# Optimization experiments

Hardware: AMD Instinct MI355X
Metric: run time of the kernel (lower is better)

Reference implementation:

```python
import jax, jax.numpy as jnp
import numpy as np

B, L, D = 4, 4096, 128
WINDOW = 64
NEG = -1e9
LN_EPS = 1e-5


def setup_inputs() -> dict:
    key = jax.random.key(0)
    ks = jax.random.split(key, 6)
    x = jax.random.normal(ks[0], (B, L, D), dtype=jnp.float32)
    # windowed adjacency with self-loops: adj[b,i,j]=1 iff |i-j| <= WINDOW
    idx = jnp.arange(L)
    band = (jnp.abs(idx[:, None] - idx[None, :]) <= WINDOW).astype(jnp.int32)
    adj = jnp.broadcast_to(band, (B, L, L))
    mask = np.ones((B, L), dtype=np.int32)
    mask[B // 2 :, -L // 8 :] = 0
    mask = jnp.asarray(mask)
    s = 1.0 / np.sqrt(D)
    Wq = jax.random.normal(ks[1], (D, D), dtype=jnp.float32) * s
    Wk = jax.random.normal(ks[2], (D, D), dtype=jnp.float32) * s
    Wv = jax.random.normal(ks[3], (D, D), dtype=jnp.float32) * s
    W_upd = jax.random.normal(ks[4], (2 * D, D), dtype=jnp.float32) * (1.0 / np.sqrt(2 * D))
    b_upd = jnp.zeros((D,), dtype=jnp.float32)
    gamma = jnp.ones((D,), dtype=jnp.float32)
    beta = jnp.zeros((D,), dtype=jnp.float32)
    return {"x": x, "adj": adj, "mask": mask, "Wq": Wq, "Wk": Wk, "Wv": Wv,
            "W_upd": W_upd, "b_upd": b_upd, "gamma": gamma, "beta": beta}


def reference(x, adj, mask, Wq, Wk, Wv, W_upd, b_upd, gamma, beta):
    d = x.shape[-1]
    q = jnp.einsum("bld,de->ble", x, Wq)
    k = jnp.einsum("bld,de->ble", x, Wk)
    v = jnp.einsum("bld,de->ble", x, Wv)
    logits = jnp.einsum("bld,bmd->blm", q, k) / jnp.sqrt(jnp.float32(d))
    logits = jnp.where(adj == 0, NEG, logits)
    logits = jnp.where(mask[:, :, None] == 0, NEG, logits)
    logits = jnp.where(mask[:, None, :] == 0, NEG, logits)
    attn = jax.nn.softmax(logits, axis=-1)  # dropout = identity (eval mode)
    agg = jnp.einsum("blm,bmd->bld", attn, v)
    h = jnp.concatenate([x, agg], axis=-1)  # [B, L, 2D]
    upd = jax.nn.relu(h @ W_upd + b_upd)
    y = x + upd
    mu = jnp.mean(y, axis=-1, keepdims=True)
    var = jnp.var(y, axis=-1, keepdims=True)
    return gamma * (y - mu) * jax.lax.rsqrt(var + LN_EPS) + beta
```

## Files before the change

kernel.cpp:

```cpp
#include <hip/hip_runtime.h>

#define BB 4
#define LL 4096
#define DD 128
#define WIN 64
#define BL (BB * LL)

#define TQ 32
#define CK 64

typedef unsigned short u16;

__device__ __forceinline__ u16 f2b(float f) {
  union { float f; unsigned int u; } x;
  x.f = f;
  unsigned int r = x.u + 0x7fffu + ((x.u >> 16) & 1u);
  return (u16)(r >> 16);
}
__device__ __forceinline__ float b2f_lo(unsigned int u) {
  union { unsigned int u; float f; } x;
  x.u = u << 16;
  return x.f;
}
__device__ __forceinline__ float b2f_hi(unsigned int u) {
  union { unsigned int u; float f; } x;
  x.u = u & 0xffff0000u;
  return x.f;
}
__device__ __forceinline__ void unpack8(uint4 u, float* f) {
  f[0] = b2f_lo(u.x); f[1] = b2f_hi(u.x);
  f[2] = b2f_lo(u.y); f[3] = b2f_hi(u.y);
  f[4] = b2f_lo(u.z); f[5] = b2f_hi(u.z);
  f[6] = b2f_lo(u.w); f[7] = b2f_hi(u.w);
}

__global__ __launch_bounds__(256) void qkv_kernel(
    const float* __restrict__ x, const float* __restrict__ Wq,
    const float* __restrict__ Wk, const float* __restrict__ Wv,
    u16* __restrict__ q, u16* __restrict__ k, u16* __restrict__ v,
    float* __restrict__ vmean_sum) {
  __shared__ float xs[32][132];
  __shared__ float ws[32][132];

  const int t = threadIdx.x;
  const int row0 = blockIdx.x * 32;
  const int tm = t >> 4;
  const int tn = t & 15;

  {
    int rr = t >> 5, d4 = t & 31;
    const float4* xg = (const float4*)(x + (size_t)row0 * DD);
    #pragma unroll
    for (int p = 0; p < 4; ++p) {
      int row = p * 8 + rr;
      ((float4*)&xs[row][0])[d4] = xg[row * 32 + d4];
    }
  }

  const float* Ws[3] = {Wq, Wk, Wv};
  u16* outs[3] = {q, k, v};

  for (int w = 0; w < 3; ++w) {
    float acc0[8], acc1[8];
    #pragma unroll
    for (int j = 0; j < 8; ++j) { acc0[j] = 0.f; acc1[j] = 0.f; }

    for (int kc = 0; kc < 4; ++kc) {
      __syncthreads();
      {
        int rr = t >> 5, d4 = t & 31;
        const float4* wg = (const float4*)(Ws[w] + (size_t)kc * 32 * DD);
        #pragma unroll
        for (int p = 0; p < 4; ++p) {
          int row = p * 8 + rr;
          ((float4*)&ws[row][0])[d4] = wg[row * 32 + d4];
        }
      }
      __syncthreads();

      #pragma unroll
      for (int k4 = 0; k4 < 8; ++k4) {
        float4 a0 = ((const float4*)&xs[tm][0])[kc * 8 + k4];
        float4 a1 = ((const float4*)&xs[tm + 16][0])[kc * 8 + k4];
        float a0c[4] = {a0.x, a0.y, a0.z, a0.w};
        float a1c[4] = {a1.x, a1.y, a1.z, a1.w};
        #pragma unroll
        for (int o = 0; o < 4; ++o) {
          int kk = k4 * 4 + o;
          float4 b0 = ((const float4*)&ws[kk][0])[tn];
          float4 b1 = ((const float4*)&ws[kk][0])[16 + tn];
          acc0[0] += a0c[o] * b0.x; acc0[1] += a0c[o] * b0.y;
          acc0[2] += a0c[o] * b0.z; acc0[3] += a0c[o] * b0.w;
          acc0[4] += a0c[o] * b1.x; acc0[5] += a0c[o] * b1.y;
          acc0[6] += a0c[o] * b1.z; acc0[7] += a0c[o] * b1.w;
          acc1[0] += a1c[o] * b0.x; acc1[1] += a1c[o] * b0.y;
          acc1[2] += a1c[o] * b0.z; acc1[3] += a1c[o] * b0.w;
          acc1[4] += a1c[o] * b1.x; acc1[5] += a1c[o] * b1.y;
          acc1[6] += a1c[o] * b1.z; acc1[7] += a1c[o] * b1.w;
        }
      }
    }

    u16* op = outs[w] + (size_t)row0 * DD;
    {
      ushort4 s;
      s.x = f2b(acc0[0]); s.y = f2b(acc0[1]); s.z = f2b(acc0[2]); s.w = f2b(acc0[3]);
      *(ushort4*)(op + (size_t)tm * DD + 4 * tn) = s;
      s.x = f2b(acc0[4]); s.y = f2b(acc0[5]); s.z = f2b(acc0[6]); s.w = f2b(acc0[7]);
      *(ushort4*)(op + (size_t)tm * DD + 64 + 4 * tn) = s;
      s.x = f2b(acc1[0]); s.y = f2b(acc1[1]); s.z = f2b(acc1[2]); s.w = f2b(acc1[3]);
      *(ushort4*)(op + (size_t)(tm + 16) * DD + 4 * tn) = s;
      s.x = f2b(acc1[4]); s.y = f2b(acc1[5]); s.z = f2b(acc1[6]); s.w = f2b(acc1[7]);
      *(ushort4*)(op + (size_t)(tm + 16) * DD + 64 + 4 * tn) = s;
    }

    if (w == 2) {
      __syncthreads();
      ((float4*)&ws[tm][0])[tn] = make_float4(acc0[0], acc0[1], acc0[2], acc0[3]);
      ((float4*)&ws[tm][0])[16 + tn] = make_float4(acc0[4], acc0[5], acc0[6], acc0[7]);
      ((float4*)&ws[tm + 16][0])[tn] = make_float4(acc1[0], acc1[1], acc1[2], acc1[3]);
      ((float4*)&ws[tm + 16][0])[16 + tn] = make_float4(acc1[4], acc1[5], acc1[6], acc1[7]);
      __syncthreads();
      if (t < DD) {
        float s = 0.f;
        #pragma unroll 8
        for (int r = 0; r < 32; ++r) s += ws[r][t];
        atomicAdd(&vmean_sum[(row0 >> 12) * DD + t], s);
      }
    }
  }
}

__global__ __launch_bounds__(128) void attn_kernel(
    const u16* __restrict__ q, const u16* __restrict__ k,
    const u16* __restrict__ v, const float* __restrict__ vmean_sum,
    const int* __restrict__ mask, float* __restrict__ agg) {
  __shared__ u16 qs[TQ][136];
  __shared__ u16 ks[CK][136];
  __shared__ float ps[TQ][66];
  __shared__ int cms[CK];

  const int bx = blockIdx.x;
  const int b = bx >> 7;
  const int i0 = (bx & 127) * TQ;
  const int t = threadIdx.x;
  const int tm = t >> 4;
  const int tn = t & 15;

  const size_t rowbase = ((size_t)b * LL + i0) * DD;

  {
    const uint4* qg = (const uint4*)(q + rowbase);
    #pragma unroll
    for (int p = 0; p < 4; ++p) {
      int row = p * 8 + tm;
      *(uint4*)&qs[row][8 * tn] = qg[row * 16 + tn];
    }
  }

  float accv[4][8];
  float lsum[4];
  #pragma unroll
  for (int m = 0; m < 4; ++m) {
    lsum[m] = 0.f;
    #pragma unroll
    for (int j = 0; j < 8; ++j) accv[m][j] = 0.f;
  }

  for (int ch = 0; ch < 3; ++ch) {
    const int j0 = i0 - WIN + ch * CK;
    __syncthreads();

    {
      #pragma unroll
      for (int p = 0; p < 8; ++p) {
        int row = p * 8 + tm;
        int j = j0 + row;
        int jc = j < 0 ? 0 : (j > LL - 1 ? LL - 1 : j);
        *(uint4*)&ks[row][8 * tn] =
            ((const uint4*)(k + ((size_t)b * LL + jc) * DD))[tn];
      }
      if (t < CK) {
        int j = j0 + t;
        cms[t] = (j >= 0 && j < LL) ? mask[b * LL + j] : 0;
      }
    }
    __syncthreads();

    float S[4][4];
    #pragma unroll
    for (int m = 0; m < 4; ++m)
      #pragma unroll
      for (int n = 0; n < 4; ++n) S[m][n] = 0.f;

    for (int k8 = 0; k8 < 16; ++k8) {
      float af[4][8], bf[4][8];
      #pragma unroll
      for (int m = 0; m < 4; ++m)
        unpack8(*(const uint4*)&qs[tm + 8 * m][8 * k8], af[m]);
      #pragma unroll
      for (int n = 0; n < 4; ++n)
        unpack8(*(const uint4*)&ks[tn + 16 * n][8 * k8], bf[n]);
      #pragma unroll
      for (int m = 0; m < 4; ++m)
        #pragma unroll
        for (int n = 0; n < 4; ++n) {
          float s = S[m][n];
          #pragma unroll
          for (int j = 0; j < 8; ++j) s += af[m][j] * bf[n][j];
          S[m][n] = s;
        }
    }

    #pragma unroll
    for (int m = 0; m < 4; ++m) {
      int iR = i0 + tm + 8 * m;
      #pragma unroll
      for (int n = 0; n < 4; ++n) {
        int col = tn + 16 * n;
        int j = j0 + col;
        int dj = iR - j;
        dj = dj < 0 ? -dj : dj;
        bool ok = (dj <= WIN) && ((unsigned)j < (unsigned)LL) && (cms[col] != 0);
        float p = ok ? __expf(S[m][n] * 0.08838834764831845f) : 0.f;
        lsum[m] += p;
        ps[tm + 8 * m][col] = p;
      }
    }
    __syncthreads();

    {
      #pragma unroll
      for (int p = 0; p < 8; ++p) {
        int row = p * 8 + tm;
        int j = j0 + row;
        int jc = j < 0 ? 0 : (j > LL - 1 ? LL - 1 : j);
        *(uint4*)&ks[row][8 * tn] =
            ((const uint4*)(v + ((size_t)b * LL + jc) * DD))[tn];
      }
    }
    __syncthreads();

    #pragma unroll 2
    for (int c = 0; c < CK; ++c) {
      float vf[8];
      unpack8(*(const uint4*)&ks[c][8 * tn], vf);
      float pm[4];
      #pragma unroll
      for (int m = 0; m < 4; ++m) pm[m] = ps[tm + 8 * m][c];
      #pragma unroll
      for (int m = 0; m < 4; ++m)
        #pragma unroll
        for (int j = 0; j < 8; ++j) accv[m][j] += pm[m] * vf[j];
    }
  }

  #pragma unroll
  for (int m = 0; m < 4; ++m) {
    float l = lsum[m];
    l += __shfl_xor(l, 1);
    l += __shfl_xor(l, 2);
    l += __shfl_xor(l, 4);
    l += __shfl_xor(l, 8);
    lsum[m] = l;
  }

  #pragma unroll
  for (int m = 0; m < 4; ++m) {
    int row = tm + 8 * m;
    int iR = i0 + row;
    float o[8];
    if (mask[b * LL + iR] != 0) {
      float inv = 1.0f / lsum[m];
      #pragma unroll
      for (int j = 0; j < 8; ++j) o[j] = accv[m][j] * inv;
    } else {
      const float s = 1.0f / LL;
      #pragma unroll
      for (int j = 0; j < 8; ++j) o[j] = vmean_sum[b * DD + 8 * tn + j] * s;
    }
    float* dst = agg + rowbase + (size_t)row * DD + 8 * tn;
    *(float4*)dst = make_float4(o[0], o[1], o[2], o[3]);
    *(float4*)(dst + 4) = make_float4(o[4], o[5], o[6], o[7]);
  }
}

__global__ __launch_bounds__(256) void mlp_ln_kernel(
    const float* __restrict__ x, const float* __restrict__ agg,
    const float* __restrict__ Wu, const float* __restrict__ bias,
    const float* __restrict__ gamma, const float* __restrict__ beta,
    float* __restrict__ out) {
  __shared__ float hs[32][36];
  __shared__ float ws[32][132];

  const int t = threadIdx.x;
  const int row0 = blockIdx.x * 32;
  const int tm = t >> 4, tn = t & 15;

  float acc0[8], acc1[8];
  #pragma unroll
  for (int j = 0; j < 8; ++j) { acc0[j] = 0.f; acc1[j] = 0.f; }

  for (int kc = 0; kc < 8; ++kc) {
    __syncthreads();
    {
      const float* src = (kc < 4) ? (x + (size_t)row0 * DD + kc * 32)
                                  : (agg + (size_t)row0 * DD + (kc - 4) * 32);
      int row = t >> 3, d4 = t & 7;
      ((float4*)&hs[row][0])[d4] = ((const float4*)(src + (size_t)row * DD))[d4];
    }
    {
      int rr = t >> 5, d4 = t & 31;
      const float4* wg = (const float4*)(Wu + (size_t)kc * 32 * DD);
      #pragma unroll
      for (int p = 0; p < 4; ++p) {
        int row = p * 8 + rr;
        ((float4*)&ws[row][0])[d4] = wg[row * 32 + d4];
      }
    }
    __syncthreads();

    #pragma unroll
    for (int k4 = 0; k4 < 8; ++k4) {
      float4 a0 = ((const float4*)&hs[tm][0])[k4];
      float4 a1 = ((const float4*)&hs[tm + 16][0])[k4];
      float a0c[4] = {a0.x, a0.y, a0.z, a0.w};
      float a1c[4] = {a1.x, a1.y, a1.z, a1.w};
      #pragma unroll
      for (int o = 0; o < 4; ++o) {
        int kk = k4 * 4 + o;
        float4 b0 = ((const float4*)&ws[kk][0])[tn];
        float4 b1 = ((const float4*)&ws[kk][0])[16 + tn];
        acc0[0] += a0c[o] * b0.x; acc0[1] += a0c[o] * b0.y;
        acc0[2] += a0c[o] * b0.z; acc0[3] += a0c[o] * b0.w;
        acc0[4] += a0c[o] * b1.x; acc0[5] += a0c[o] * b1.y;
        acc0[6] += a0c[o] * b1.z; acc0[7] += a0c[o] * b1.w;
        acc1[0] += a1c[o] * b0.x; acc1[1] += a1c[o] * b0.y;
        acc1[2] += a1c[o] * b0.z; acc1[3] += a1c[o] * b0.w;
        acc1[4] += a1c[o] * b1.x; acc1[5] += a1c[o] * b1.y;
        acc1[6] += a1c[o] * b1.z; acc1[7] += a1c[o] * b1.w;
      }
    }
  }

  const float4 bv0 = ((const float4*)bias)[tn];
  const float4 bv1 = ((const float4*)bias)[16 + tn];
  const float4 g0 = ((const float4*)gamma)[tn];
  const float4 g1 = ((const float4*)gamma)[16 + tn];
  const float4 be0 = ((const float4*)beta)[tn];
  const float4 be1 = ((const float4*)beta)[16 + tn];

  #pragma unroll
  for (int m = 0; m < 2; ++m) {
    const float* accp0 = m ? acc1 : acc0;
    int row = tm + 16 * m;
    const float4 xr0 = ((const float4*)(x + (size_t)(row0 + row) * DD))[tn];
    const float4 xr1 = ((const float4*)(x + (size_t)(row0 + row) * DD))[16 + tn];
    float y[8];
    y[0] = xr0.x + fmaxf(accp0[0] + bv0.x, 0.f);
    y[1] = xr0.y + fmaxf(accp0[1] + bv0.y, 0.f);
    y[2] = xr0.z + fmaxf(accp0[2] + bv0.z, 0.f);
    y[3] = xr0.w + fmaxf(accp0[3] + bv0.w, 0.f);
    y[4] = xr1.x + fmaxf(accp0[4] + bv1.x, 0.f);
    y[5] = xr1.y + fmaxf(accp0[5] + bv1.y, 0.f);
    y[6] = xr1.z + fmaxf(accp0[6] + bv1.z, 0.f);
    y[7] = xr1.w + fmaxf(accp0[7] + bv1.w, 0.f);
    float s = 0.f, ss = 0.f;
    #pragma unroll
    for (int j = 0; j < 8; ++j) { s += y[j]; ss += y[j] * y[j]; }
    s += __shfl_xor(s, 1); ss += __shfl_xor(ss, 1);
    s += __shfl_xor(s, 2); ss += __shfl_xor(ss, 2);
    s += __shfl_xor(s, 4); ss += __shfl_xor(ss, 4);
    s += __shfl_xor(s, 8); ss += __shfl_xor(ss, 8);
    float mu = s * (1.0f / DD);
    float var = ss * (1.0f / DD) - mu * mu;
    float rstd = rsqrtf(var + 1e-5f);
    float4 o0 = make_float4(g0.x * ((y[0] - mu) * rstd) + be0.x,
                            g0.y * ((y[1] - mu) * rstd) + be0.y,
                            g0.z * ((y[2] - mu) * rstd) + be0.z,
                            g0.w * ((y[3] - mu) * rstd) + be0.w);
    float4 o1 = make_float4(g1.x * ((y[4] - mu) * rstd) + be1.x,
                            g1.y * ((y[5] - mu) * rstd) + be1.y,
                            g1.z * ((y[6] - mu) * rstd) + be1.z,
                            g1.w * ((y[7] - mu) * rstd) + be1.w);
    ((float4*)(out + (size_t)(row0 + row) * DD))[tn] = o0;
    ((float4*)(out + (size_t)(row0 + row) * DD))[16 + tn] = o1;
  }
}

extern "C" void kernel_launch(void* const* d_in, const int* in_sizes, int n_in,
                              void* d_out, int out_size, void* d_ws,
                              size_t ws_size, hipStream_t stream) {
  const float* x = (const float*)d_in[0];
  const int* mask = (const int*)d_in[2];
  const float* Wq = (const float*)d_in[3];
  const float* Wk = (const float*)d_in[4];
  const float* Wv = (const float*)d_in[5];
  const float* Wu = (const float*)d_in[6];
  const float* bias = (const float*)d_in[7];
  const float* gamma = (const float*)d_in[8];
  const float* beta = (const float*)d_in[9];
  float* out = (float*)d_out;

  float* agg = (float*)d_ws;
  u16* q = (u16*)(agg + (size_t)BL * DD);
  u16* k = q + (size_t)BL * DD;
  u16* v = k + (size_t)BL * DD;
  float* vmean_sum = (float*)(v + (size_t)BL * DD);

  hipMemsetAsync(vmean_sum, 0, BB * DD * sizeof(float), stream);

  qkv_kernel<<<BL / 32, 256, 0, stream>>>(x, Wq, Wk, Wv, q, k, v, vmean_sum);
  attn_kernel<<<BL / TQ, 128, 0, stream>>>(q, k, v, vmean_sum, mask, agg);
  mlp_ln_kernel<<<BL / 32, 256, 0, stream>>>(x, agg, Wu, bias, gamma, beta,
                                             out);
}
```

Before: 429.9 us.

## Restructure QKV, attention and MLP kernels to read weights directly and stage K/V together

The QKV kernel now launches one grid slice per projection over 64-row tiles and reads weights straight from global memory (through cache) instead of staging them in shared memory. The attention kernel loads K and V into separate shared buffers in a single pass and stores probabilities transposed, cutting one sync and one reload per chunk. The MLP/LayerNorm kernel stages the full concatenated [x, agg] row block once and also reads weights from global memory. This removes shared-memory weight tiling and the barriers around it. In exchange it relies on L1/L2 for weight reuse and uses more shared memory per attention block.

```diff
diff --git a/kernel.cpp b/kernel.cpp
--- a/kernel.cpp
+++ b/kernel.cpp
@@ -5,9 +5,7 @@
 #define DD 128
 #define WIN 64
 #define BL (BB * LL)
-
 #define TQ 32
-#define CK 64
 
 typedef unsigned short u16;
 
@@ -33,100 +31,81 @@
   f[4] = b2f_lo(u.z); f[5] = b2f_hi(u.z);
   f[6] = b2f_lo(u.w); f[7] = b2f_hi(u.w);
 }
+__device__ __forceinline__ float comp4(float4 a, int d) {
+  return d == 0 ? a.x : (d == 1 ? a.y : (d == 2 ? a.z : a.w));
+}
 
 __global__ __launch_bounds__(256) void qkv_kernel(
     const float* __restrict__ x, const float* __restrict__ Wq,
     const float* __restrict__ Wk, const float* __restrict__ Wv,
     u16* __restrict__ q, u16* __restrict__ k, u16* __restrict__ v,
     float* __restrict__ vmean_sum) {
-  __shared__ float xs[32][132];
-  __shared__ float ws[32][132];
+  __shared__ float xs[64][132];
 
   const int t = threadIdx.x;
-  const int row0 = blockIdx.x * 32;
-  const int tm = t >> 4;
-  const int tn = t & 15;
+  const int row0 = blockIdx.x * 64;
+  const int which = blockIdx.y;
+  const float* __restrict__ W = which == 0 ? Wq : (which == 1 ? Wk : Wv);
+  u16* __restrict__ outp = which == 0 ? q : (which == 1 ? k : v);
 
   {
-    int rr = t >> 5, d4 = t & 31;
     const float4* xg = (const float4*)(x + (size_t)row0 * DD);
     #pragma unroll
-    for (int p = 0; p < 4; ++p) {
-      int row = p * 8 + rr;
-      ((float4*)&xs[row][0])[d4] = xg[row * 32 + d4];
-    }
-  }
-
-  const float* Ws[3] = {Wq, Wk, Wv};
-  u16* outs[3] = {q, k, v};
-
-  for (int w = 0; w < 3; ++w) {
-    float acc0[8], acc1[8];
-    #pragma unroll
-    for (int j = 0; j < 8; ++j) { acc0[j] = 0.f; acc1[j] = 0.f; }
-
-    for (int kc = 0; kc < 4; ++kc) {
-      __syncthreads();
-      {
-        int rr = t >> 5, d4 = t & 31;
-        const float4* wg = (const float4*)(Ws[w] + (size_t)kc * 32 * DD);
-        #pragma unroll
-        for (int p = 0; p < 4; ++p) {
-          int row = p * 8 + rr;
-          ((float4*)&ws[row][0])[d4] = wg[row * 32 + d4];
-        }
-      }
-      __syncthreads();
-
-      #pragma unroll
-      for (int k4 = 0; k4 < 8; ++k4) {
-        float4 a0 = ((const float4*)&xs[tm][0])[kc * 8 + k4];
-        float4 a1 = ((const float4*)&xs[tm + 16][0])[kc * 8 + k4];
-        float a0c[4] = {a0.x, a0.y, a0.z, a0.w};
-        float a1c[4] = {a1.x, a1.y, a1.z, a1.w};
-        #pragma unroll
-        for (int o = 0; o < 4; ++o) {
-          int kk = k4 * 4 + o;
-          float4 b0 = ((const float4*)&ws[kk][0])[tn];
-          float4 b1 = ((const float4*)&ws[kk][0])[16 + tn];
-          acc0[0] += a0c[o] * b0.x; acc0[1] += a0c[o] * b0.y;
-          acc0[2] += a0c[o] * b0.z; acc0[3] += a0c[o] * b0.w;
-          acc0[4] += a0c[o] * b1.x; acc0[5] += a0c[o] * b1.y;
-          acc0[6] += a0c[o] * b1.z; acc0[7] += a0c[o] * b1.w;
-          acc1[0] += a1c[o] * b0.x; acc1[1] += a1c[o] * b0.y;
-          acc1[2] += a1c[o] * b0.z; acc1[3] += a1c[o] * b0.w;
-          acc1[4] += a1c[o] * b1.x; acc1[5] += a1c[o] * b1.y;
-          acc1[6] += a1c[o] * b1.z; acc1[7] += a1c[o] * b1.w;
-        }
-      }
-    }
-
-    u16* op = outs[w] + (size_t)row0 * DD;
-    {
-      ushort4 s;
-      s.x = f2b(acc0[0]); s.y = f2b(acc0[1]); s.z = f2b(acc0[2]); s.w = f2b(acc0[3]);
-      *(ushort4*)(op + (size_t)tm * DD + 4 * tn) = s;
-      s.x = f2b(acc0[4]); s.y = f2b(acc0[5]); s.z = f2b(acc0[6]); s.w = f2b(acc0[7]);
-      *(ushort4*)(op + (size_t)tm * DD + 64 + 4 * tn) = s;
-      s.x = f2b(acc1[0]); s.y = f2b(acc1[1]); s.z = f2b(acc1[2]); s.w = f2b(acc1[3]);
-      *(ushort4*)(op + (size_t)(tm + 16) * DD + 4 * tn) = s;
-      s.x = f2b(acc1[4]); s.y = f2b(acc1[5]); s.z = f2b(acc1[6]); s.w = f2b(acc1[7]);
-      *(ushort4*)(op + (size_t)(tm + 16) * DD + 64 + 4 * tn) = s;
-    }
-
-    if (w == 2) {
-      __syncthreads();
-      ((float4*)&ws[tm][0])[tn] = make_float4(acc0[0], acc0[1], acc0[2], acc0[3]);
-      ((float4*)&ws[tm][0])[16 + tn] = make_float4(acc0[4], acc0[5], acc0[6], acc0[7]);
-      ((float4*)&ws[tm + 16][0])[tn] = make_float4(acc1[0], acc1[1], acc1[2], acc1[3]);
-      ((float4*)&ws[tm + 16][0])[16 + tn] = make_float4(acc1[4], acc1[5], acc1[6], acc1[7]);
-      __syncthreads();
-      if (t < DD) {
-        float s = 0.f;
-        #pragma unroll 8
-        for (int r = 0; r < 32; ++r) s += ws[r][t];
-        atomicAdd(&vmean_sum[(row0 >> 12) * DD + t], s);
-      }
+    for (int p = 0; p < 8; ++p) {
+      int idx = t + 256 * p;
+      ((float4*)&xs[idx >> 5][0])[idx & 31] = xg[idx];
+    }
+  }
+  __syncthreads();
+
+  const int rg = t >> 5;
+  const int cg = t & 31;
+  const float4* W4 = (const float4*)W;
+
+  float4 acc[8];
+  #pragma unroll
+  for (int m = 0; m < 8; ++m) acc[m] = make_float4(0.f, 0.f, 0.f, 0.f);
+
+  #pragma unroll 2
+  for (int k4 = 0; k4 < 32; ++k4) {
+    float4 a[8];
+    #pragma unroll
+    for (int m = 0; m < 8; ++m)
+      a[m] = ((const float4*)&xs[rg + 8 * m][0])[k4];
+    #pragma unroll
+    for (int d = 0; d < 4; ++d) {
+      float4 w = W4[(size_t)(k4 * 4 + d) * 32 + cg];
+      #pragma unroll
+      for (int m = 0; m < 8; ++m) {
+        float av = comp4(a[m], d);
+        acc[m].x += av * w.x; acc[m].y += av * w.y;
+        acc[m].z += av * w.z; acc[m].w += av * w.w;
+      }
+    }
+  }
+
+  #pragma unroll
+  for (int m = 0; m < 8; ++m) {
+    ushort4 s;
+    s.x = f2b(acc[m].x); s.y = f2b(acc[m].y);
+    s.z = f2b(acc[m].z); s.w = f2b(acc[m].w);
+    *(ushort4*)(outp + (size_t)(row0 + rg + 8 * m) * DD + 4 * cg) = s;
+  }
+
+  if (which == 2) {
+    __syncthreads();
+    float4 cs = make_float4(0.f, 0.f, 0.f, 0.f);
+    #pragma unroll
+    for (int m = 0; m < 8; ++m) {
+      cs.x += acc[m].x; cs.y += acc[m].y; cs.z += acc[m].z; cs.w += acc[m].w;
+    }
+    ((float4*)&xs[rg][0])[cg] = cs;
+    __syncthreads();
+    if (t < DD) {
+      float s = 0.f;
+      #pragma unroll
+      for (int r = 0; r < 8; ++r) s += xs[r][t];
+      atomicAdd(&vmean_sum[(row0 >> 12) * DD + t], s);
     }
   }
 }
@@ -136,9 +115,11 @@
     const u16* __restrict__ v, const float* __restrict__ vmean_sum,
     const int* __restrict__ mask, float* __restrict__ agg) {
   __shared__ u16 qs[TQ][136];
-  __shared__ u16 ks[CK][136];
-  __shared__ float ps[TQ][66];
-  __shared__ int cms[CK];
+  __shared__ u16 ks[64][136];
+  __shared__ u16 vs[64][136];
+  __shared__ float pt[64][36];
+  __shared__ float rowsum[TQ];
+  __shared__ int cms[64];
 
   const int bx = blockIdx.x;
   const int b = bx >> 7;
@@ -153,8 +134,8 @@
     const uint4* qg = (const uint4*)(q + rowbase);
     #pragma unroll
     for (int p = 0; p < 4; ++p) {
-      int row = p * 8 + tm;
-      *(uint4*)&qs[row][8 * tn] = qg[row * 16 + tn];
+      int idx = t + 128 * p;
+      *(uint4*)&qs[idx >> 4][8 * (idx & 15)] = qg[idx];
     }
   }
 
@@ -168,19 +149,22 @@
   }
 
   for (int ch = 0; ch < 3; ++ch) {
-    const int j0 = i0 - WIN + ch * CK;
+    const int j0 = i0 - WIN + ch * 64;
     __syncthreads();
 
     {
+      const uint4* kg = (const uint4*)(k + (size_t)b * LL * DD);
+      const uint4* vg = (const uint4*)(v + (size_t)b * LL * DD);
       #pragma unroll
       for (int p = 0; p < 8; ++p) {
-        int row = p * 8 + tm;
+        int idx = t + 128 * p;
+        int row = idx >> 4, c = idx & 15;
         int j = j0 + row;
         int jc = j < 0 ? 0 : (j > LL - 1 ? LL - 1 : j);
-        *(uint4*)&ks[row][8 * tn] =
-            ((const uint4*)(k + ((size_t)b * LL + jc) * DD))[tn];
-      }
-      if (t < CK) {
+        *(uint4*)&ks[row][8 * c] = kg[(size_t)jc * 16 + c];
+        *(uint4*)&vs[row][8 * c] = vg[(size_t)jc * 16 + c];
+      }
+      if (t < 64) {
         int j = j0 + t;
         cms[t] = (j >= 0 && j < LL) ? mask[b * LL + j] : 0;
       }
@@ -214,7 +198,8 @@
 
     #pragma unroll
     for (int m = 0; m < 4; ++m) {
-      int iR = i0 + tm + 8 * m;
+      int row = tm + 8 * m;
+      int iR = i0 + row;
       #pragma unroll
       for (int n = 0; n < 4; ++n) {
         int col = tn + 16 * n;
@@ -224,34 +209,21 @@
         bool ok = (dj <= WIN) && ((unsigned)j < (unsigned)LL) && (cms[col] != 0);
         float p = ok ? __expf(S[m][n] * 0.08838834764831845f) : 0.f;
         lsum[m] += p;
-        ps[tm + 8 * m][col] = p;
-      }
-    }
-    __syncthreads();
-
-    {
-      #pragma unroll
-      for (int p = 0; p < 8; ++p) {
-        int row = p * 8 + tm;
-        int j = j0 + row;
-        int jc = j < 0 ? 0 : (j > LL - 1 ? LL - 1 : j);
-        *(uint4*)&ks[row][8 * tn] =
-            ((const uint4*)(v + ((size_t)b * LL + jc) * DD))[tn];
+        pt[col][row] = p;
       }
     }
     __syncthreads();
 
     #pragma unroll 2
-    for (int c = 0; c < CK; ++c) {
+    for (int c = 0; c < 64; ++c) {
+      float4 pv = *(const float4*)&pt[c][4 * tm];
       float vf[8];
-      unpack8(*(const uint4*)&ks[c][8 * tn], vf);
-      float pm[4];
-      #pragma unroll
-      for (int m = 0; m < 4; ++m) pm[m] = ps[tm + 8 * m][c];
-      #pragma unroll
-      for (int m = 0; m < 4; ++m)
+      unpack8(*(const uint4*)&vs[c][8 * tn], vf);
+      float pr[4] = {pv.x, pv.y, pv.z, pv.w};
+      #pragma unroll
+      for (int r = 0; r < 4; ++r)
         #pragma unroll
-        for (int j = 0; j < 8; ++j) accv[m][j] += pm[m] * vf[j];
+        for (int j = 0; j < 8; ++j) accv[r][j] += pr[r] * vf[j];
     }
   }
 
@@ -262,18 +234,19 @@
     l += __shfl_xor(l, 2);
     l += __shfl_xor(l, 4);
     l += __shfl_xor(l, 8);
-    lsum[m] = l;
-  }
-
-  #pragma unroll
-  for (int m = 0; m < 4; ++m) {
-    int row = tm + 8 * m;
+    if (tn == 0) rowsum[tm + 8 * m] = l;
+  }
+  __syncthreads();
+
+  #pragma unroll
+  for (int r = 0; r < 4; ++r) {
+    int row = 4 * tm + r;
     int iR = i0 + row;
     float o[8];
     if (mask[b * LL + iR] != 0) {
-      float inv = 1.0f / lsum[m];
-      #pragma unroll
-      for (int j = 0; j < 8; ++j) o[j] = accv[m][j] * inv;
+      float inv = 1.0f / rowsum[row];
+      #pragma unroll
+      for (int j = 0; j < 8; ++j) o[j] = accv[r][j] * inv;
     } else {
       const float s = 1.0f / LL;
       #pragma unroll
@@ -290,101 +263,76 @@
     const float* __restrict__ Wu, const float* __restrict__ bias,
     const float* __restrict__ gamma, const float* __restrict__ beta,
     float* __restrict__ out) {
-  __shared__ float hs[32][36];
-  __shared__ float ws[32][132];
+  __shared__ float hs[32][264];
 
   const int t = threadIdx.x;
   const int row0 = blockIdx.x * 32;
-  const int tm = t >> 4, tn = t & 15;
-
-  float acc0[8], acc1[8];
-  #pragma unroll
-  for (int j = 0; j < 8; ++j) { acc0[j] = 0.f; acc1[j] = 0.f; }
-
-  for (int kc = 0; kc < 8; ++kc) {
-    __syncthreads();
-    {
-      const float* src = (kc < 4) ? (x + (size_t)row0 * DD + kc * 32)
-                                  : (agg + (size_t)row0 * DD + (kc - 4) * 32);
-      int row = t >> 3, d4 = t & 7;
-      ((float4*)&hs[row][0])[d4] = ((const float4*)(src + (size_t)row * DD))[d4];
-    }
-    {
-      int rr = t >> 5, d4 = t & 31;
-      const float4* wg = (const float4*)(Wu + (size_t)kc * 32 * DD);
-      #pragma unroll
-      for (int p = 0; p < 4; ++p) {
-        int row = p * 8 + rr;
-        ((float4*)&ws[row][0])[d4] = wg[row * 32 + d4];
-      }
-    }
-    __syncthreads();
-
-    #pragma unroll
-    for (int k4 = 0; k4 < 8; ++k4) {
-      float4 a0 = ((const float4*)&hs[tm][0])[k4];
-      float4 a1 = ((const float4*)&hs[tm + 16][0])[k4];
-      float a0c[4] = {a0.x, a0.y, a0.z, a0.w};
-      float a1c[4] = {a1.x, a1.y, a1.z, a1.w};
-      #pragma unroll
-      for (int o = 0; o < 4; ++o) {
-        int kk = k4 * 4 + o;
-        float4 b0 = ((const float4*)&ws[kk][0])[tn];
-        float4 b1 = ((const float4*)&ws[kk][0])[16 + tn];
-        acc0[0] += a0c[o] * b0.x; acc0[1] += a0c[o] * b0.y;
-        acc0[2] += a0c[o] * b0.z; acc0[3] += a0c[o] * b0.w;
-        acc0[4] += a0c[o] * b1.x; acc0[5] += a0c[o] * b1.y;
-        acc0[6] += a0c[o] * b1.z; acc0[7] += a0c[o] * b1.w;
-        acc1[0] += a1c[o] * b0.x; acc1[1] += a1c[o] * b0.y;
-        acc1[2] += a1c[o] * b0.z; acc1[3] += a1c[o] * b0.w;
-        acc1[4] += a1c[o] * b1.x; acc1[5] += a1c[o] * b1.y;
-        acc1[6] += a1c[o] * b1.z; acc1[7] += a1c[o] * b1.w;
-      }
-    }
-  }
-
-  const float4 bv0 = ((const float4*)bias)[tn];
-  const float4 bv1 = ((const float4*)bias)[16 + tn];
-  const float4 g0 = ((const float4*)gamma)[tn];
-  const float4 g1 = ((const float4*)gamma)[16 + tn];
-  const float4 be0 = ((const float4*)beta)[tn];
-  const float4 be1 = ((const float4*)beta)[16 + tn];
-
-  #pragma unroll
-  for (int m = 0; m < 2; ++m) {
-    const float* accp0 = m ? acc1 : acc0;
-    int row = tm + 16 * m;
-    const float4 xr0 = ((const float4*)(x + (size_t)(row0 + row) * DD))[tn];
-    const float4 xr1 = ((const float4*)(x + (size_t)(row0 + row) * DD))[16 + tn];
-    float y[8];
-    y[0] = xr0.x + fmaxf(accp0[0] + bv0.x, 0.f);
-    y[1] = xr0.y + fmaxf(accp0[1] + bv0.y, 0.f);
-    y[2] = xr0.z + fmaxf(accp0[2] + bv0.z, 0.f);
-    y[3] = xr0.w + fmaxf(accp0[3] + bv0.w, 0.f);
-    y[4] = xr1.x + fmaxf(accp0[4] + bv1.x, 0.f);
-    y[5] = xr1.y + fmaxf(accp0[5] + bv1.y, 0.f);
-    y[6] = xr1.z + fmaxf(accp0[6] + bv1.z, 0.f);
-    y[7] = xr1.w + fmaxf(accp0[7] + bv1.w, 0.f);
-    float s = 0.f, ss = 0.f;
-    #pragma unroll
-    for (int j = 0; j < 8; ++j) { s += y[j]; ss += y[j] * y[j]; }
-    s += __shfl_xor(s, 1); ss += __shfl_xor(ss, 1);
-    s += __shfl_xor(s, 2); ss += __shfl_xor(ss, 2);
-    s += __shfl_xor(s, 4); ss += __shfl_xor(ss, 4);
-    s += __shfl_xor(s, 8); ss += __shfl_xor(ss, 8);
+  const int rg = t >> 5;
+  const int cg = t & 31;
+
+  {
+    const float4* x4 = (const float4*)(x + (size_t)row0 * DD);
+    const float4* a4 = (const float4*)(agg + (size_t)row0 * DD);
+    #pragma unroll
+    for (int p = 0; p < 8; ++p) {
+      int idx = t + 256 * p;
+      int row = idx >> 6, c4 = idx & 63;
+      ((float4*)&hs[row][0])[c4] =
+          (c4 < 32) ? x4[row * 32 + c4] : a4[row * 32 + (c4 - 32)];
+    }
+  }
+  __syncthreads();
+
+  float4 acc[4];
+  #pragma unroll
+  for (int r = 0; r < 4; ++r) acc[r] = make_float4(0.f, 0.f, 0.f, 0.f);
+  const float4* Wu4 = (const float4*)Wu;
+
+  #pragma unroll 2
+  for (int k4 = 0; k4 < 64; ++k4) {
+    float4 a[4];
+    #pragma unroll
+    for (int r = 0; r < 4; ++r)
+      a[r] = ((const float4*)&hs[4 * rg + r][0])[k4];
+    #pragma unroll
+    for (int d = 0; d < 4; ++d) {
+      float4 w = Wu4[(size_t)(k4 * 4 + d) * 32 + cg];
+      #pragma unroll
+      for (int r = 0; r < 4; ++r) {
+        float av = comp4(a[r], d);
+        acc[r].x += av * w.x; acc[r].y += av * w.y;
+        acc[r].z += av * w.z; acc[r].w += av * w.w;
+      }
+    }
+  }
+
+  const float4 bv = ((const float4*)bias)[cg];
+  const float4 g = ((const float4*)gamma)[cg];
+  const float4 be = ((const float4*)beta)[cg];
+
+  #pragma unroll
+  for (int r = 0; r < 4; ++r) {
+    int row = 4 * rg + r;
+    float4 xr = ((const float4*)&hs[row][0])[cg];
+    float y0 = xr.x + fmaxf(acc[r].x + bv.x, 0.f);
+    float y1 = xr.y + fmaxf(acc[r].y + bv.y, 0.f);
+    float y2 = xr.z + fmaxf(acc[r].z + bv.z, 0.f);
+    float y3 = xr.w + fmaxf(acc[r].w + bv.w, 0.f);
+    float s = y0 + y1 + y2 + y3;
+    float ss = y0 * y0 + y1 * y1 + y2 * y2 + y3 * y3;
+    #pragma unroll
+    for (int off = 16; off > 0; off >>= 1) {
+      s += __shfl_xor(s, off);
+      ss += __shfl_xor(ss, off);
+    }
     float mu = s * (1.0f / DD);
     float var = ss * (1.0f / DD) - mu * mu;
     float rstd = rsqrtf(var + 1e-5f);
-    float4 o0 = make_float4(g0.x * ((y[0] - mu) * rstd) + be0.x,
-                            g0.y * ((y[1] - mu) * rstd) + be0.y,
-                            g0.z * ((y[2] - mu) * rstd) + be0.z,
-                            g0.w * ((y[3] - mu) * rstd) + be0.w);
-    float4 o1 = make_float4(g1.x * ((y[4] - mu) * rstd) + be1.x,
-                            g1.y * ((y[5] - mu) * rstd) + be1.y,
-                            g1.z * ((y[6] - mu) * rstd) + be1.z,
-                            g1.w * ((y[7] - mu) * rstd) + be1.w);
-    ((float4*)(out + (size_t)(row0 + row) * DD))[tn] = o0;
-    ((float4*)(out + (size_t)(row0 + row) * DD))[16 + tn] = o1;
+    float4 o = make_float4(g.x * ((y0 - mu) * rstd) + be.x,
+                           g.y * ((y1 - mu) * rstd) + be.y,
+                           g.z * ((y2 - mu) * rstd) + be.z,
+                           g.w * ((y3 - mu) * rstd) + be.w);
+    ((float4*)(out + (size_t)(row0 + row) * DD))[cg] = o;
   }
 }
 
@@ -410,7 +358,8 @@
 
   hipMemsetAsync(vmean_sum, 0, BB * DD * sizeof(float), stream);
 
-  qkv_kernel<<<BL / 32, 256, 0, stream>>>(x, Wq, Wk, Wv, q, k, v, vmean_sum);
+  qkv_kernel<<<dim3(BL / 64, 3), 256, 0, stream>>>(x, Wq, Wk, Wv, q, k, v,
+                                                   vmean_sum);
   attn_kernel<<<BL / TQ, 128, 0, stream>>>(q, k, v, vmean_sum, mask, agg);
   mlp_ln_kernel<<<BL / 32, 256, 0, stream>>>(x, agg, Wu, bias, gamma, beta,
                                              out);
```

After: 416.9 us. 3.0% less time.
